# Kernel optimization log

Measured on AMD Instinct MI355X. Metric: run time of the kernel, lower is better.

## Reference

```python
import jax, jax.numpy as jnp
import numpy as np
from jax import lax

STRIDES = (2, 2)
PADDING = 'same'  # matches init_kwargs


def _tconv_pad(k, s, padding):
    """Per-dim (lo, hi) padding so conv_general_dilated with lhs_dilation=s
    reproduces tf.nn.conv2d_transpose with the given padding mode."""
    if padding == 'valid':
        return (k - 1, k - 1)  # 'full' padding; out = (in-1)*s + k
    pt_fwd = max(k - s, 0) // 2          # top pad of the corresponding forward SAME conv
    pb = k - 1 - pt_fwd
    pa = (k + s - 2) - pb                # total transpose pad = k + s - 2; out = in*s
    return (pb, pa)


def setup_inputs() -> dict:
    key = jax.random.key(0)
    k_in, k_dw, k_pw = jax.random.split(key, 3)
    B, H, W, C = 16, 64, 64, 256
    KH = KW = 4
    D = 1          # depth_multiplier
    F = 256        # filters
    inputs = jax.random.normal(k_in, (B, H, W, C), dtype=jnp.float32)
    dw_kernel = jax.random.normal(k_dw, (KH, KW, C, D), dtype=jnp.float32) * 0.05
    pw_kernel = jax.random.normal(k_pw, (1, 1, C * D, F), dtype=jnp.float32) * 0.05
    bias = jnp.zeros((F,), dtype=jnp.float32)
    return {"inputs": inputs, "dw_kernel": dw_kernel, "pw_kernel": pw_kernel, "bias": bias}


def reference(inputs, dw_kernel, pw_kernel, bias):
    # Depthwise transposed conv. The original builds a dense (k,k,Cin*D,Cin)
    # kernel with an identity mask; mathematically that equals a grouped
    # transposed conv with groups=Cin, implemented here as a lhs-dilated
    # grouped conv with the spatially flipped depthwise kernel.
    kh, kw, cin, dm = dw_kernel.shape
    sh, sw = STRIDES
    # HWIO with I=1, O=cin*dm (channel order c*dm + d matches the masked-dense kernel)
    ker = jnp.flip(dw_kernel, (0, 1)).reshape(kh, kw, 1, cin * dm)
    pad = (_tconv_pad(kh, sh, PADDING), _tconv_pad(kw, sw, PADDING))
    x = lax.conv_general_dilated(
        inputs, ker,
        window_strides=(1, 1), padding=pad, lhs_dilation=(sh, sw),
        dimension_numbers=('NHWC', 'HWIO', 'NHWC'),
        feature_group_count=cin)  # [B, H*sh, W*sw, cin*dm] for SAME
    # 1x1 pointwise conv + bias + relu (fused elementwise tail)
    pw = pw_kernel[0, 0]                         # (cin*dm, filters)
    x = jnp.einsum('bhwc,cf->bhwf', x, pw)
    return jax.nn.relu(x + bias)
```

## Files before the change

kernel.cpp:

```cpp
#include <hip/hip_runtime.h>
#include <hip/hip_bf16.h>

#define BB 16
#define HH 64
#define WW 64
#define CC 256
#define OH 128
#define OW 128
#define FF 256

typedef __attribute__((ext_vector_type(8))) short bf16x8;
typedef __attribute__((ext_vector_type(4))) float f32x4;

__device__ __forceinline__ short f2bf(float x) {
    union { float f; unsigned u; } v; v.f = x;
    unsigned r = v.u + 0x7fffu + ((v.u >> 16) & 1u);
    return (short)(r >> 16);
}

__device__ __forceinline__ unsigned cvtpk(float lo, float hi) {
    unsigned r;
    asm("v_cvt_pk_bf16_f32 %0, %1, %2" : "=v"(r) : "v"(lo), "v"(hi));
    return r;
}

__global__ void prep_kernel(const float* __restrict__ pw, const float* __restrict__ dw,
                            short* __restrict__ pwtF, float* __restrict__ dwb) {
    if (blockIdx.x < 32) {
        const int e    = blockIdx.x * 256 + threadIdx.x;
        const int lane = e & 63;
        const int ni   = (e >> 6) & 3;
        const int kk   = (e >> 8) & 7;
        const int wc   = e >> 11;
        const int f    = wc * 64 + ni * 16 + (lane & 15);
        const int c0   = kk * 32 + (lane >> 4) * 8;
        bf16x8 v;
        #pragma unroll
        for (int j = 0; j < 8; ++j) v[j] = f2bf(pw[(size_t)(c0 + j) * FF + f]);
        reinterpret_cast<bf16x8*>(pwtF)[e] = v;
    } else {
        for (int k = threadIdx.x; k < 4 * 4 * CC; k += 256) {
            int r = k >> 10;
            int rem = k & 1023;
            int s = rem >> 8;
            int c = rem & 255;
            dwb[(r * CC + c) * 4 + s] = dw[(r * 4 + s) * CC + c];
        }
    }
}

__device__ __forceinline__ void tap(float acc[8], const float w[8], const float* xptr) {
    const float4* xp = reinterpret_cast<const float4*>(xptr);
    float4 x0 = xp[0], x1 = xp[1];
    acc[0] += w[0] * x0.x; acc[1] += w[1] * x0.y;
    acc[2] += w[2] * x0.z; acc[3] += w[3] * x0.w;
    acc[4] += w[4] * x1.x; acc[5] += w[5] * x1.y;
    acc[6] += w[6] * x1.z; acc[7] += w[7] * x1.w;
}

__global__ __launch_bounds__(512, 4)
void sepconvt_kernel(const float* __restrict__ X,
                     const float* __restrict__ dwb,
                     const short* __restrict__ pwtF,
                     const float* __restrict__ bias,
                     float* __restrict__ out) {
    __shared__ bf16x8 t_lds[2][32 * 32];

    const int tid  = threadIdx.x;
    const int wid  = tid >> 6;
    const int lane = tid & 63;
    const bool producer = (wid < 4);
    const int blk  = blockIdx.x;
    const int oh = blk & (OH - 1);
    const int b  = blk >> 7;

    int r0, r1, i0, i1;
    if (oh & 1) { r0 = 0; i0 = (oh + 1) >> 1; r1 = 2; i1 = (oh - 1) >> 1; }
    else        { r0 = 1; i0 = oh >> 1;       r1 = 3; i1 = (oh >> 1) - 1; }

    if (producer) {
        const int cg  = tid & 31;
        const int c0  = cg << 3;
        const int owp = (tid >> 5) & 7;
        const int par = owp & 1;

        float w[2][2][8];
        const float4* dwb4 = reinterpret_cast<const float4*>(dwb);
        #pragma unroll
        for (int e = 0; e < 8; ++e) {
            float4 wa = dwb4[r0 * CC + c0 + e];
            float4 wb = dwb4[r1 * CC + c0 + e];
            w[0][0][e] = par ? wa.x : wa.y;
            w[0][1][e] = par ? wa.z : wa.w;
            w[1][0][e] = par ? wb.x : wb.y;
            w[1][1][e] = par ? wb.z : wb.w;
        }

        const bool va0 = (unsigned)i0 < HH;
        const bool va1 = (unsigned)i1 < HH;
        const float* Xr0 = X + (size_t)(b * HH + (va0 ? i0 : 0)) * WW * CC;
        const float* Xr1 = X + (size_t)(b * HH + (va1 ? i1 : 0)) * WW * CC;

        #pragma unroll
        for (int q = 0; q < 4; ++q) {
            const int qb = q & 1;
            #pragma unroll
            for (int h = 0; h < 4; ++h) {
                const int owl = owp + h * 8;
                const int ow  = q * 32 + owl;
                int je, jo;
                if (par) { je = (ow + 1) >> 1; jo = (ow - 1) >> 1; }
                else     { je = ow >> 1;       jo = (ow >> 1) - 1; }
                const bool vje = (unsigned)je < WW;
                const bool vjo = (unsigned)jo < WW;

                float acc[8];
                #pragma unroll
                for (int e = 0; e < 8; ++e) acc[e] = 0.f;

                if (va0) {
                    if (vje) tap(acc, w[0][0], Xr0 + je * CC + c0);
                    if (vjo) tap(acc, w[0][1], Xr0 + jo * CC + c0);
                }
                if (va1) {
                    if (vje) tap(acc, w[1][0], Xr1 + je * CC + c0);
                    if (vjo) tap(acc, w[1][1], Xr1 + jo * CC + c0);
                }

                union { unsigned u[4]; bf16x8 v; } pk;
                pk.u[0] = cvtpk(acc[0], acc[1]);
                pk.u[1] = cvtpk(acc[2], acc[3]);
                pk.u[2] = cvtpk(acc[4], acc[5]);
                pk.u[3] = cvtpk(acc[6], acc[7]);
                t_lds[qb][owl * 32 + (cg ^ (owl & 7))] = pk.v;
            }
            __syncthreads();
        }
    } else {
        const int wc  = wid - 4;
        const int lr  = lane & 15;
        const int lk8 = lane >> 4;
        const bf16x8* pvF = reinterpret_cast<const bf16x8*>(pwtF) + (size_t)wc * 2048 + lane;

        f32x4 bv[4];
        #pragma unroll
        for (int ni = 0; ni < 4; ++ni)
            bv[ni] = *reinterpret_cast<const f32x4*>(&bias[wc * 64 + ni * 16 + lk8 * 4]);

        #pragma unroll
        for (int q = 0; q < 4; ++q) {
            __syncthreads();
            const int qb = q & 1;

            f32x4 acc[2][4];
            #pragma unroll
            for (int mi = 0; mi < 2; ++mi)
                #pragma unroll
                for (int ni = 0; ni < 4; ++ni)
                    acc[mi][ni] = (f32x4){0.f, 0.f, 0.f, 0.f};

            #pragma unroll
            for (int kk = 0; kk < 8; ++kk) {
                const int kg = kk * 4 + lk8;
                bf16x8 af[2], bfr[4];
                #pragma unroll
                for (int mi = 0; mi < 2; ++mi) {
                    const int row = mi * 16 + lr;
                    af[mi] = t_lds[qb][row * 32 + (kg ^ (row & 7))];
                }
                #pragma unroll
                for (int ni = 0; ni < 4; ++ni)
                    bfr[ni] = pvF[(kk * 4 + ni) * 64];
                #pragma unroll
                for (int mi = 0; mi < 2; ++mi)
                    #pragma unroll
                    for (int ni = 0; ni < 4; ++ni)
                        acc[mi][ni] = __builtin_amdgcn_mfma_f32_16x16x32_bf16(
                            bfr[ni], af[mi], acc[mi][ni], 0, 0, 0);
            }

            float* obase = out + ((size_t)(b * OH + oh) * OW + q * 32) * FF;
            #pragma unroll
            for (int ni = 0; ni < 4; ++ni) {
                const int f0 = wc * 64 + ni * 16 + lk8 * 4;
                #pragma unroll
                for (int mi = 0; mi < 2; ++mi) {
                    const int ow = mi * 16 + lr;
                    f32x4 v = acc[mi][ni] + bv[ni];
                    v[0] = v[0] > 0.f ? v[0] : 0.f;
                    v[1] = v[1] > 0.f ? v[1] : 0.f;
                    v[2] = v[2] > 0.f ? v[2] : 0.f;
                    v[3] = v[3] > 0.f ? v[3] : 0.f;
                    *reinterpret_cast<f32x4*>(&obase[(size_t)ow * FF + f0]) = v;
                }
            }
        }
    }
}

extern "C" void kernel_launch(void* const* d_in, const int* in_sizes, int n_in,
                              void* d_out, int out_size, void* d_ws, size_t ws_size,
                              hipStream_t stream) {
    (void)in_sizes; (void)n_in; (void)out_size; (void)ws_size;
    const float* X    = (const float*)d_in[0];
    const float* dw   = (const float*)d_in[1];
    const float* pw   = (const float*)d_in[2];
    const float* bias = (const float*)d_in[3];
    float* out = (float*)d_out;
    short* pwtF = (short*)d_ws;
    float* dwb  = (float*)((char*)d_ws + 131072);

    prep_kernel<<<dim3(33), dim3(256), 0, stream>>>(pw, dw, pwtF, dwb);
    sepconvt_kernel<<<dim3(BB * OH), dim3(512), 0, stream>>>(X, dwb, pwtF, bias, out);
}
```

Baseline: 150.3 us.

## Reuse input columns across adjacent outputs via sliding window in depthwise producer

Each producer thread now handles a contiguous run of same-parity output columns and keeps the previous input column in registers. Every input pixel is loaded once per thread instead of twice, and validity branches are replaced by zeroed weights and clamped indices. This cuts global/L2 load traffic and branching in the producer stage, at the cost of more registers for the carried column and a changed mapping of threads to LDS rows.

```diff
diff --git a/kernel.cpp b/kernel.cpp
--- a/kernel.cpp
+++ b/kernel.cpp
@@ -49,15 +49,6 @@
     }
 }
 
-__device__ __forceinline__ void tap(float acc[8], const float w[8], const float* xptr) {
-    const float4* xp = reinterpret_cast<const float4*>(xptr);
-    float4 x0 = xp[0], x1 = xp[1];
-    acc[0] += w[0] * x0.x; acc[1] += w[1] * x0.y;
-    acc[2] += w[2] * x0.z; acc[3] += w[3] * x0.w;
-    acc[4] += w[4] * x1.x; acc[5] += w[5] * x1.y;
-    acc[6] += w[6] * x1.z; acc[7] += w[7] * x1.w;
-}
-
 __global__ __launch_bounds__(512, 4)
 void sepconvt_kernel(const float* __restrict__ X,
                      const float* __restrict__ dwb,
@@ -82,7 +73,11 @@
         const int cg  = tid & 31;
         const int c0  = cg << 3;
         const int owp = (tid >> 5) & 7;
-        const int par = owp & 1;
+        const int p   = owp & 1;
+        const int seg = owp >> 1;
+
+        const bool va0 = (unsigned)i0 < HH;
+        const bool va1 = (unsigned)i1 < HH;
 
         float w[2][2][8];
         const float4* dwb4 = reinterpret_cast<const float4*>(dwb);
@@ -90,49 +85,67 @@
         for (int e = 0; e < 8; ++e) {
             float4 wa = dwb4[r0 * CC + c0 + e];
             float4 wb = dwb4[r1 * CC + c0 + e];
-            w[0][0][e] = par ? wa.x : wa.y;
-            w[0][1][e] = par ? wa.z : wa.w;
-            w[1][0][e] = par ? wb.x : wb.y;
-            w[1][1][e] = par ? wb.z : wb.w;
-        }
-
-        const bool va0 = (unsigned)i0 < HH;
-        const bool va1 = (unsigned)i1 < HH;
+            w[0][0][e] = va0 ? (p ? wa.x : wa.y) : 0.f;
+            w[0][1][e] = va0 ? (p ? wa.z : wa.w) : 0.f;
+            w[1][0][e] = va1 ? (p ? wb.x : wb.y) : 0.f;
+            w[1][1][e] = va1 ? (p ? wb.z : wb.w) : 0.f;
+        }
+
         const float* Xr0 = X + (size_t)(b * HH + (va0 ? i0 : 0)) * WW * CC;
         const float* Xr1 = X + (size_t)(b * HH + (va1 ? i1 : 0)) * WW * CC;
 
         #pragma unroll
         for (int q = 0; q < 4; ++q) {
             const int qb = q & 1;
-            #pragma unroll
-            for (int h = 0; h < 4; ++h) {
-                const int owl = owp + h * 8;
-                const int ow  = q * 32 + owl;
-                int je, jo;
-                if (par) { je = (ow + 1) >> 1; jo = (ow - 1) >> 1; }
-                else     { je = ow >> 1;       jo = (ow >> 1) - 1; }
-                const bool vje = (unsigned)je < WW;
-                const bool vjo = (unsigned)jo < WW;
+            const int j0 = q * 16 + seg * 4 + p;
+
+            float xp0[8], xp1[8];
+            {
+                const int cm1 = (j0 > 0) ? (j0 - 1) : 0;
+                const float4* a0 = reinterpret_cast<const float4*>(Xr0 + cm1 * CC + c0);
+                const float4* a1 = reinterpret_cast<const float4*>(Xr1 + cm1 * CC + c0);
+                float4 u0 = a0[0], u1 = a0[1], v0 = a1[0], v1 = a1[1];
+                if (q == 0 && j0 == 0) {
+                    u0 = u1 = v0 = v1 = (float4){0.f, 0.f, 0.f, 0.f};
+                }
+                xp0[0]=u0.x; xp0[1]=u0.y; xp0[2]=u0.z; xp0[3]=u0.w;
+                xp0[4]=u1.x; xp0[5]=u1.y; xp0[6]=u1.z; xp0[7]=u1.w;
+                xp1[0]=v0.x; xp1[1]=v0.y; xp1[2]=v0.z; xp1[3]=v0.w;
+                xp1[4]=v1.x; xp1[5]=v1.y; xp1[6]=v1.z; xp1[7]=v1.w;
+            }
+
+            #pragma unroll
+            for (int k = 0; k < 4; ++k) {
+                const int jc = j0 + k;
+                const int jcc = (jc < WW) ? jc : (WW - 1);
+                const float4* a0 = reinterpret_cast<const float4*>(Xr0 + jcc * CC + c0);
+                const float4* a1 = reinterpret_cast<const float4*>(Xr1 + jcc * CC + c0);
+                float4 u0 = a0[0], u1 = a0[1], v0 = a1[0], v1 = a1[1];
+                if (k == 3 && q == 3 && jc >= WW) {
+                    u0 = u1 = v0 = v1 = (float4){0.f, 0.f, 0.f, 0.f};
+                }
+                float xc0[8], xc1[8];
+                xc0[0]=u0.x; xc0[1]=u0.y; xc0[2]=u0.z; xc0[3]=u0.w;
+                xc0[4]=u1.x; xc0[5]=u1.y; xc0[6]=u1.z; xc0[7]=u1.w;
+                xc1[0]=v0.x; xc1[1]=v0.y; xc1[2]=v0.z; xc1[3]=v0.w;
+                xc1[4]=v1.x; xc1[5]=v1.y; xc1[6]=v1.z; xc1[7]=v1.w;
 
                 float acc[8];
                 #pragma unroll
-                for (int e = 0; e < 8; ++e) acc[e] = 0.f;
-
-                if (va0) {
-                    if (vje) tap(acc, w[0][0], Xr0 + je * CC + c0);
-                    if (vjo) tap(acc, w[0][1], Xr0 + jo * CC + c0);
-                }
-                if (va1) {
-                    if (vje) tap(acc, w[1][0], Xr1 + je * CC + c0);
-                    if (vjo) tap(acc, w[1][1], Xr1 + jo * CC + c0);
-                }
+                for (int e = 0; e < 8; ++e)
+                    acc[e] = w[0][0][e] * xc0[e] + w[0][1][e] * xp0[e]
+                           + w[1][0][e] * xc1[e] + w[1][1][e] * xp1[e];
 
                 union { unsigned u[4]; bf16x8 v; } pk;
                 pk.u[0] = cvtpk(acc[0], acc[1]);
                 pk.u[1] = cvtpk(acc[2], acc[3]);
                 pk.u[2] = cvtpk(acc[4], acc[5]);
                 pk.u[3] = cvtpk(acc[6], acc[7]);
+                const int owl = seg * 8 + p + 2 * k;
                 t_lds[qb][owl * 32 + (cg ^ (owl & 7))] = pk.v;
+
+                #pragma unroll
+                for (int e = 0; e < 8; ++e) { xp0[e] = xc0[e]; xp1[e] = xc1[e]; }
             }
             __syncthreads();
         }
```

Result: no change. 148.5 us (-1.2%).

## Stage input rows into LDS via async global_load_lds with double-buffered producer pipeline

Applied to the files above, without the earlier changes.

Producer waves now copy the needed input columns for each 32-wide output chunk into a 96KB LDS buffer with global_load_lds, prefetching the next chunk while computing the current one. Neighbouring outputs reuse the staged columns from registers, and each lane handles 4 channels. Depthwise weights are read directly and zeroed for invalid rows, which drops the dw reshuffle from the prep kernel. Barriers become raw s_barrier with manual waitcnt. The large LDS footprint lowers occupancy (launch bounds 4→2 blocks), and the manual sync is fragile.

```diff
diff --git a/kernel.cpp b/kernel.cpp
--- a/kernel.cpp
+++ b/kernel.cpp
@@ -24,52 +24,32 @@
     return r;
 }
 
-__global__ void prep_kernel(const float* __restrict__ pw, const float* __restrict__ dw,
-                            short* __restrict__ pwtF, float* __restrict__ dwb) {
-    if (blockIdx.x < 32) {
-        const int e    = blockIdx.x * 256 + threadIdx.x;
-        const int lane = e & 63;
-        const int ni   = (e >> 6) & 3;
-        const int kk   = (e >> 8) & 7;
-        const int wc   = e >> 11;
-        const int f    = wc * 64 + ni * 16 + (lane & 15);
-        const int c0   = kk * 32 + (lane >> 4) * 8;
-        bf16x8 v;
-        #pragma unroll
-        for (int j = 0; j < 8; ++j) v[j] = f2bf(pw[(size_t)(c0 + j) * FF + f]);
-        reinterpret_cast<bf16x8*>(pwtF)[e] = v;
-    } else {
-        for (int k = threadIdx.x; k < 4 * 4 * CC; k += 256) {
-            int r = k >> 10;
-            int rem = k & 1023;
-            int s = rem >> 8;
-            int c = rem & 255;
-            dwb[(r * CC + c) * 4 + s] = dw[(r * 4 + s) * CC + c];
-        }
-    }
-}
-
-__device__ __forceinline__ void tap(float acc[8], const float w[8], const float* xptr) {
-    const float4* xp = reinterpret_cast<const float4*>(xptr);
-    float4 x0 = xp[0], x1 = xp[1];
-    acc[0] += w[0] * x0.x; acc[1] += w[1] * x0.y;
-    acc[2] += w[2] * x0.z; acc[3] += w[3] * x0.w;
-    acc[4] += w[4] * x1.x; acc[5] += w[5] * x1.y;
-    acc[6] += w[6] * x1.z; acc[7] += w[7] * x1.w;
-}
-
-__global__ __launch_bounds__(512, 4)
+__global__ void prep_kernel(const float* __restrict__ pw, short* __restrict__ pwtF) {
+    const int e    = blockIdx.x * 256 + threadIdx.x;
+    const int lane = e & 63;
+    const int ni   = (e >> 6) & 3;
+    const int kk   = (e >> 8) & 7;
+    const int wc   = e >> 11;
+    const int f    = wc * 64 + ni * 16 + (lane & 15);
+    const int c0   = kk * 32 + (lane >> 4) * 8;
+    bf16x8 v;
+    #pragma unroll
+    for (int j = 0; j < 8; ++j) v[j] = f2bf(pw[(size_t)(c0 + j) * FF + f]);
+    reinterpret_cast<bf16x8*>(pwtF)[e] = v;
+}
+
+__global__ __launch_bounds__(512, 2)
 void sepconvt_kernel(const float* __restrict__ X,
-                     const float* __restrict__ dwb,
+                     const float* __restrict__ dw,
                      const short* __restrict__ pwtF,
                      const float* __restrict__ bias,
                      float* __restrict__ out) {
+    __shared__ __align__(16) char xraw[98304];
     __shared__ bf16x8 t_lds[2][32 * 32];
 
     const int tid  = threadIdx.x;
     const int wid  = tid >> 6;
     const int lane = tid & 63;
-    const bool producer = (wid < 4);
     const int blk  = blockIdx.x;
     const int oh = blk & (OH - 1);
     const int b  = blk >> 7;
@@ -77,64 +57,110 @@
     int r0, r1, i0, i1;
     if (oh & 1) { r0 = 0; i0 = (oh + 1) >> 1; r1 = 2; i1 = (oh - 1) >> 1; }
     else        { r0 = 1; i0 = oh >> 1;       r1 = 3; i1 = (oh >> 1) - 1; }
-
-    if (producer) {
-        const int cg  = tid & 31;
-        const int c0  = cg << 3;
-        const int owp = (tid >> 5) & 7;
-        const int par = owp & 1;
-
-        float w[2][2][8];
-        const float4* dwb4 = reinterpret_cast<const float4*>(dwb);
-        #pragma unroll
-        for (int e = 0; e < 8; ++e) {
-            float4 wa = dwb4[r0 * CC + c0 + e];
-            float4 wb = dwb4[r1 * CC + c0 + e];
-            w[0][0][e] = par ? wa.x : wa.y;
-            w[0][1][e] = par ? wa.z : wa.w;
-            w[1][0][e] = par ? wb.x : wb.y;
-            w[1][1][e] = par ? wb.z : wb.w;
+    const bool va0 = (unsigned)i0 < HH;
+    const bool va1 = (unsigned)i1 < HH;
+
+    if (wid < 4) {
+        const int w  = wid;
+        const int c4 = lane << 2;
+        const float* Xr0 = X + (size_t)(b * HH + (va0 ? i0 : 0)) * WW * CC + c4;
+        const float* Xr1 = X + (size_t)(b * HH + (va1 ? i1 : 0)) * WW * CC + c4;
+
+        float4 wt[2][2][2];
+        {
+            const float4 z = {0.f, 0.f, 0.f, 0.f};
+            #pragma unroll
+            for (int r = 0; r < 2; ++r) {
+                const int rr = r ? r1 : r0;
+                const bool va = r ? va1 : va0;
+                float4 s0 = *reinterpret_cast<const float4*>(dw + (rr * 4 + 0) * CC + c4);
+                float4 s1 = *reinterpret_cast<const float4*>(dw + (rr * 4 + 1) * CC + c4);
+                float4 s2 = *reinterpret_cast<const float4*>(dw + (rr * 4 + 2) * CC + c4);
+                float4 s3 = *reinterpret_cast<const float4*>(dw + (rr * 4 + 3) * CC + c4);
+                wt[r][0][0] = va ? s1 : z;
+                wt[r][0][1] = va ? s3 : z;
+                wt[r][1][0] = va ? s0 : z;
+                wt[r][1][1] = va ? s2 : z;
+            }
         }
 
-        const bool va0 = (unsigned)i0 < HH;
-        const bool va1 = (unsigned)i1 < HH;
-        const float* Xr0 = X + (size_t)(b * HH + (va0 ? i0 : 0)) * WW * CC;
-        const float* Xr1 = X + (size_t)(b * HH + (va1 ? i1 : 0)) * WW * CC;
-
+        auto STAGE = [&](int q, int qb) {
+            const int W0  = q * 32 + w * 8;
+            const int jlo = (W0 >> 1) - 1;
+            const int base = qb * 49152 + w * 12288;
+            #pragma unroll
+            for (int ci = 0; ci < 6; ++ci) {
+                int j = jlo + ci;
+                j = j < 0 ? 0 : (j > WW - 1 ? WW - 1 : j);
+                __builtin_amdgcn_global_load_lds(
+                    (const __attribute__((address_space(1))) unsigned*)(Xr0 + (size_t)j * CC),
+                    (__attribute__((address_space(3))) unsigned*)(xraw + base + ci * 1024),
+                    16, 0, 0);
+                __builtin_amdgcn_global_load_lds(
+                    (const __attribute__((address_space(1))) unsigned*)(Xr1 + (size_t)j * CC),
+                    (__attribute__((address_space(3))) unsigned*)(xraw + base + 6144 + ci * 1024),
+                    16, 0, 0);
+            }
+        };
+
+        auto LC = [&](const char* xw, int ci, float4& x0, float4& x1) {
+            x0 = *reinterpret_cast<const float4*>(xw + ci * 1024 + lane * 16);
+            x1 = *reinterpret_cast<const float4*>(xw + 6144 + ci * 1024 + lane * 16);
+        };
+
+        auto EMIT = [&](int qb, int owl, int p,
+                        const float4& xe0, const float4& xe1,
+                        const float4& xo0, const float4& xo1) {
+            const float4 we0 = wt[0][p][0], wo0 = wt[0][p][1];
+            const float4 we1 = wt[1][p][0], wo1 = wt[1][p][1];
+            float a0 = we0.x * xe0.x + wo0.x * xo0.x + we1.x * xe1.x + wo1.x * xo1.x;
+            float a1 = we0.y * xe0.y + wo0.y * xo0.y + we1.y * xe1.y + wo1.y * xo1.y;
+            float a2 = we0.z * xe0.z + wo0.z * xo0.z + we1.z * xe1.z + wo1.z * xo1.z;
+            float a3 = we0.w * xe0.w + wo0.w * xo0.w + we1.w * xe1.w + wo1.w * xo1.w;
+            unsigned* dst = reinterpret_cast<unsigned*>(
+                reinterpret_cast<char*>(&t_lds[qb][0]) + owl * 512 +
+                (((lane >> 1) ^ (owl & 7)) << 4) + ((lane & 1) << 3));
+            dst[0] = cvtpk(a0, a1);
+            dst[1] = cvtpk(a2, a3);
+        };
+
+        auto PRODUCE = [&](int q, int qb) {
+            const char* xw = xraw + qb * 49152 + w * 12288;
+            const int W0 = q * 32 + w * 8;
+            const int o0 = w * 8;
+            float4 xo0, xo1, xe0, xe1;
+            LC(xw, 0, xo0, xo1);
+            LC(xw, 1, xe0, xe1);
+            if (W0 == 0) { xo0 = (float4){0,0,0,0}; xo1 = (float4){0,0,0,0}; }
+            EMIT(qb, o0 + 0, 0, xe0, xe1, xo0, xo1);
+            xo0 = xe0; xo1 = xe1; LC(xw, 2, xe0, xe1);
+            EMIT(qb, o0 + 1, 1, xe0, xe1, xo0, xo1);
+            EMIT(qb, o0 + 2, 0, xe0, xe1, xo0, xo1);
+            xo0 = xe0; xo1 = xe1; LC(xw, 3, xe0, xe1);
+            EMIT(qb, o0 + 3, 1, xe0, xe1, xo0, xo1);
+            EMIT(qb, o0 + 4, 0, xe0, xe1, xo0, xo1);
+            xo0 = xe0; xo1 = xe1; LC(xw, 4, xe0, xe1);
+            EMIT(qb, o0 + 5, 1, xe0, xe1, xo0, xo1);
+            EMIT(qb, o0 + 6, 0, xe0, xe1, xo0, xo1);
+            xo0 = xe0; xo1 = xe1; LC(xw, 5, xe0, xe1);
+            if (W0 == 120) { xe0 = (float4){0,0,0,0}; xe1 = (float4){0,0,0,0}; }
+            EMIT(qb, o0 + 7, 1, xe0, xe1, xo0, xo1);
+        };
+
+        STAGE(0, 0);
         #pragma unroll
         for (int q = 0; q < 4; ++q) {
-            const int qb = q & 1;
-            #pragma unroll
-            for (int h = 0; h < 4; ++h) {
-                const int owl = owp + h * 8;
-                const int ow  = q * 32 + owl;
-                int je, jo;
-                if (par) { je = (ow + 1) >> 1; jo = (ow - 1) >> 1; }
-                else     { je = ow >> 1;       jo = (ow >> 1) - 1; }
-                const bool vje = (unsigned)je < WW;
-                const bool vjo = (unsigned)jo < WW;
-
-                float acc[8];
-                #pragma unroll
-                for (int e = 0; e < 8; ++e) acc[e] = 0.f;
-
-                if (va0) {
-                    if (vje) tap(acc, w[0][0], Xr0 + je * CC + c0);
-                    if (vjo) tap(acc, w[0][1], Xr0 + jo * CC + c0);
-                }
-                if (va1) {
-                    if (vje) tap(acc, w[1][0], Xr1 + je * CC + c0);
-                    if (vjo) tap(acc, w[1][1], Xr1 + jo * CC + c0);
-                }
-
-                union { unsigned u[4]; bf16x8 v; } pk;
-                pk.u[0] = cvtpk(acc[0], acc[1]);
-                pk.u[1] = cvtpk(acc[2], acc[3]);
-                pk.u[2] = cvtpk(acc[4], acc[5]);
-                pk.u[3] = cvtpk(acc[6], acc[7]);
-                t_lds[qb][owl * 32 + (cg ^ (owl & 7))] = pk.v;
-            }
-            __syncthreads();
+            if (q < 3) {
+                STAGE(q + 1, (q + 1) & 1);
+                asm volatile("s_waitcnt vmcnt(12)" ::: "memory");
+            } else {
+                asm volatile("s_waitcnt vmcnt(0)" ::: "memory");
+            }
+            __builtin_amdgcn_sched_barrier(0);
+            PRODUCE(q, q & 1);
+            asm volatile("s_waitcnt lgkmcnt(0)" ::: "memory");
+            __builtin_amdgcn_sched_barrier(0);
+            asm volatile("s_barrier" ::: "memory");
         }
     } else {
         const int wc  = wid - 4;
@@ -149,7 +175,8 @@
 
         #pragma unroll
         for (int q = 0; q < 4; ++q) {
-            __syncthreads();
+            asm volatile("s_barrier" ::: "memory");
+            __builtin_amdgcn_sched_barrier(0);
             const int qb = q & 1;
 
             f32x4 acc[2][4];
@@ -208,8 +235,7 @@
     const float* bias = (const float*)d_in[3];
     float* out = (float*)d_out;
     short* pwtF = (short*)d_ws;
-    float* dwb  = (float*)((char*)d_ws + 131072);
-
-    prep_kernel<<<dim3(33), dim3(256), 0, stream>>>(pw, dw, pwtF, dwb);
-    sepconvt_kernel<<<dim3(BB * OH), dim3(512), 0, stream>>>(X, dwb, pwtF, bias, out);
-}
+
+    prep_kernel<<<dim3(32), dim3(256), 0, stream>>>(pw, pwtF);
+    sepconvt_kernel<<<dim3(BB * OH), dim3(512), 0, stream>>>(X, dw, pwtF, bias, out);
+}
```

Result: faster. 126.2 us, median of 4 (-16.1%).
